# Kernel optimization log

Hardware: AMD Instinct MI355X
Metric: run time of the kernel (lower is better)

Reference implementation:

```python
import jax, jax.numpy as jnp
import numpy as np

DIM = 768
NH = 12
HID = int(DIM * 1.5)  # 1152
B_, T_, W_ = 8, 8, 14
HW = 14 * 14
N = HW + 1
BT = B_ * T_


def _ln(x, g, b, eps=1e-5):
    m = jnp.mean(x, axis=-1, keepdims=True)
    v = jnp.var(x, axis=-1, keepdims=True)
    return (x - m) / jnp.sqrt(v + eps) * g + b


def _attn(x, wqkv, wproj, bproj, nh):
    # manual q@k^T -> softmax -> @v, as in the torch module (no qkv bias)
    b, n, c = x.shape
    hd = c // nh
    scale = hd ** -0.5
    qkv = (x @ wqkv.T).reshape(b, n, 3, nh, hd).transpose(2, 0, 3, 1, 4)
    q, k, v = qkv[0], qkv[1], qkv[2]
    a = jax.nn.softmax(jnp.einsum('bhnd,bhmd->bhnm', q, k) * scale, axis=-1)
    o = jnp.einsum('bhnm,bhmd->bhnd', a, v).transpose(0, 2, 1, 3).reshape(b, n, c)
    return o @ wproj.T + bproj


def setup_inputs() -> dict:
    key = jax.random.key(0)
    ks = jax.random.split(key, 16)
    s = 0.02
    d = {
        'x': jax.random.normal(ks[0], (BT, N, DIM), jnp.float32),
        'ln1_g': jnp.ones((DIM,), jnp.float32),
        'ln1_b': jnp.zeros((DIM,), jnp.float32),
        'qkv_w': jax.random.normal(ks[1], (3 * DIM, DIM), jnp.float32) * s,
        'proj_w': jax.random.normal(ks[2], (DIM, DIM), jnp.float32) * s,
        'proj_b': jnp.zeros((DIM,), jnp.float32),
        'tln_g': jnp.ones((DIM,), jnp.float32),
        'tln_b': jnp.zeros((DIM,), jnp.float32),
        'tqkv_w': jax.random.normal(ks[3], (3 * DIM, DIM), jnp.float32) * s,
        'tproj_w': jax.random.normal(ks[4], (DIM, DIM), jnp.float32) * s,
        'tproj_b': jnp.zeros((DIM,), jnp.float32),
        # module zero-inits temporal_fc; use small random so the branch is exercised
        'tfc_w': jax.random.normal(ks[5], (DIM, DIM), jnp.float32) * s,
        'tfc_b': jnp.zeros((DIM,), jnp.float32),
        'ln2_g': jnp.ones((DIM,), jnp.float32),
        'ln2_b': jnp.zeros((DIM,), jnp.float32),
        'fc1_w': jax.random.normal(ks[6], (HID, DIM), jnp.float32) * s,
        'fc1_b': jnp.zeros((HID,), jnp.float32),
        'fc2_w': jax.random.normal(ks[7], (DIM, HID), jnp.float32) * s,
        'fc2_b': jnp.zeros((DIM,), jnp.float32),
        'B': B_, 'T': T_, 'W': W_,
    }
    return d


def reference(x, ln1_g, ln1_b, qkv_w, proj_w, proj_b,
              tln_g, tln_b, tqkv_w, tproj_w, tproj_b, tfc_w, tfc_b,
              ln2_g, ln2_b, fc1_w, fc1_b, fc2_w, fc2_b, B, T, W):
    bt, n, c = x.shape
    hw = n - 1  # spatial tokens (cls excluded)
    # temporal branch: (b t) hw m -> (b hw) t m
    xt = x[:, 1:, :].reshape(B, T, hw, c).transpose(0, 2, 1, 3).reshape(B * hw, T, c)
    xt = _attn(_ln(xt, tln_g, tln_b), tqkv_w, tproj_w, tproj_b, NH)
    xt = xt.reshape(B, hw, T, c).transpose(0, 2, 1, 3).reshape(bt, hw, c)
    xt = xt @ tfc_w.T + tfc_b
    x = x.at[:, 1:, :].add(xt)  # in-place += in torch
    # spatial attention + residual
    x = x + _attn(_ln(x, ln1_g, ln1_b), qkv_w, proj_w, proj_b, NH)
    # MLP + residual (exact GELU, matching nn.GELU default)
    h = jax.nn.gelu(_ln(x, ln2_g, ln2_b) @ fc1_w.T + fc1_b, approximate=False)
    x = x + (h @ fc2_w.T + fc2_b)
    return x
```

## Files before the change

kernel.cpp:

```cpp
#include <hip/hip_runtime.h>
#include <hip/hip_bf16.h>


#define DIM   768
#define NH    12
#define HD    64
#define HID   1152
#define HIDP  1280
#define B_    8
#define T_    8
#define HW_   196
#define NTOK  197
#define BT_   64
#define MROWS (BT_ * NTOK)
#define TROWS (B_ * HW_ * T_)

typedef __bf16 bf16x8 __attribute__((ext_vector_type(8)));
typedef float  f32x4  __attribute__((ext_vector_type(4)));

__device__ inline float bf2f(ushort u) { return __uint_as_float(((unsigned)u) << 16); }
__device__ inline ushort f2bf(float f) {
    unsigned u = __float_as_uint(f);
    unsigned r = (u + 0x7fffu + ((u >> 16) & 1u)) >> 16;
    return (ushort)r;
}

__device__ inline float wred_sum(float v) {
    #pragma unroll
    for (int m = 32; m; m >>= 1) v += __shfl_xor(v, m);
    return v;
}

__device__ __forceinline__ void gload_lds16(const void* g, void* l) {
    __builtin_amdgcn_global_load_lds(
        (const __attribute__((address_space(1))) unsigned int*)g,
        (__attribute__((address_space(3))) unsigned int*)l, 16, 0, 0);
}

__device__ __forceinline__ int xcd_lin(int gid, int nwg) {
    int q = nwg >> 3, r = nwg & 7;
    int xcd = gid & 7, idx = gid >> 3;
    return (xcd < r ? xcd * (q + 1) : r * (q + 1) + (xcd - r) * q) + idx;
}

#define MFMA16(a, b, c) __builtin_amdgcn_mfma_f32_16x16x32_bf16(a, b, c, 0, 0, 0)

#define PREP_T0 576
#define PREP_T1 (PREP_T0 + 192)
#define PREP_T2 (PREP_T1 + TROWS / 4)
#define FL_DD8  73728
#define FL_C0   (3 * FL_DD8)
#define FL_C1   (FL_C0 + FL_DD8)
#define FL_C2   (FL_C1 + 3 * FL_DD8)
#define FL_C3   (FL_C2 + FL_DD8)
#define FL_C4   (FL_C3 + HID * DIM / 8)
#define FL_C5   (FL_C4 + (HIDP - HID) * DIM / 8)
#define FL_C6   (FL_C5 + DIM * HIDP / 8)
#define FL_C7   (FL_C6 + HIDP / 8)
#define FL_C8   (FL_C7 + BT_ * DIM / 8)
#define PREP_GRID (PREP_T2 + (FL_C8 + 255) / 256)

__global__ __launch_bounds__(256) void prep(
    const float* __restrict__ x, const float* __restrict__ tln_g, const float* __restrict__ tln_b,
    const float* __restrict__ qkv_w, const float* __restrict__ proj_w,
    const float* __restrict__ tqkv_w, const float* __restrict__ tproj_w,
    const float* __restrict__ tproj_b, const float* __restrict__ tfc_wf,
    const float* __restrict__ tfc_b, const float* __restrict__ fc1_w,
    const float* __restrict__ fc1_b, const float* __restrict__ fc2_w,
    ushort* __restrict__ w_qkv, ushort* __restrict__ w_proj,
    ushort* __restrict__ w_tqkv, ushort* __restrict__ w_tfc,
    ushort* __restrict__ tprojT, ushort* __restrict__ w_fc1p,
    ushort* __restrict__ w_fc2p, float* __restrict__ fc1_bp,
    float* __restrict__ b_comb, ushort* __restrict__ bufA, float* __restrict__ out)
{
    __shared__ float tsm[32][33];
    int b = blockIdx.x, tid = threadIdx.x;

    if (b < PREP_T0) {
        int bx = b % 24, by = b / 24;
        int lx = tid & 31, ly = tid >> 5;
        #pragma unroll
        for (int i = 0; i < 32; i += 8)
            tsm[ly + i][lx] = tproj_w[(size_t)(by * 32 + ly + i) * DIM + bx * 32 + lx];
        __syncthreads();
        #pragma unroll
        for (int i = 0; i < 32; i += 8)
            tprojT[(size_t)(bx * 32 + ly + i) * DIM + by * 32 + lx] = f2bf(tsm[lx][ly + i]);
        return;
    }
    if (b < PREP_T1) {
        int w = (b - PREP_T0) * 4 + (tid >> 6), lane = tid & 63;
        float s = 0.f;
        for (int j = lane; j < DIM; j += 64) s += tfc_wf[(size_t)w * DIM + j] * tproj_b[j];
        s = wred_sum(s);
        if (lane == 0) b_comb[w] = s + tfc_b[w];
        return;
    }
    if (b < PREP_T2) {
        int widx = tid >> 6, lane = tid & 63;
        int r = (b - PREP_T1) * 4 + widx;
        int t = r & 7, pp = (r >> 3) % HW_, bb = r / (HW_ * T_);
        const float* row = x + ((size_t)(bb * T_ + t) * NTOK + 1 + pp) * DIM;
        float v[12], sum = 0.f, sq = 0.f;
        #pragma unroll
        for (int c = 0; c < 3; ++c) {
            float4 t4 = *(const float4*)(row + c * 256 + lane * 4);
            v[c*4+0] = t4.x; v[c*4+1] = t4.y; v[c*4+2] = t4.z; v[c*4+3] = t4.w;
            sum += t4.x + t4.y + t4.z + t4.w;
            sq  += t4.x*t4.x + t4.y*t4.y + t4.z*t4.z + t4.w*t4.w;
        }
        sum = wred_sum(sum); sq = wred_sum(sq);
        float mean = sum * (1.f / DIM);
        float var  = sq * (1.f / DIM) - mean * mean;
        float rstd = rsqrtf(var + 1e-5f);
        #pragma unroll
        for (int c = 0; c < 3; ++c) {
            int idx = c * 256 + lane * 4;
            float4 gg = *(const float4*)(tln_g + idx);
            float4 bb2 = *(const float4*)(tln_b + idx);
            ushort4 o;
            o.x = f2bf((v[c*4+0] - mean) * rstd * gg.x + bb2.x);
            o.y = f2bf((v[c*4+1] - mean) * rstd * gg.y + bb2.y);
            o.z = f2bf((v[c*4+2] - mean) * rstd * gg.z + bb2.z);
            o.w = f2bf((v[c*4+3] - mean) * rstd * gg.w + bb2.w);
            *(ushort4*)(bufA + (size_t)r * DIM + idx) = o;
        }
        return;
    }

    int i = (b - PREP_T2) * 256 + tid;
    if (i >= FL_C8) return;
    if (i < FL_C4) {
        const float* s; ushort* d; int base;
        if      (i < FL_C0) { s = qkv_w;  d = w_qkv;  base = 0;     }
        else if (i < FL_C1) { s = proj_w; d = w_proj; base = FL_C0; }
        else if (i < FL_C2) { s = tqkv_w; d = w_tqkv; base = FL_C1; }
        else if (i < FL_C3) { s = tfc_wf; d = w_tfc;  base = FL_C2; }
        else                { s = fc1_w;  d = w_fc1p; base = FL_C3; }
        int k = i - base;
        float4 a = *(const float4*)(s + (size_t)k * 8);
        float4 bb = *(const float4*)(s + (size_t)k * 8 + 4);
        ushort o[8] = {f2bf(a.x), f2bf(a.y), f2bf(a.z), f2bf(a.w),
                       f2bf(bb.x), f2bf(bb.y), f2bf(bb.z), f2bf(bb.w)};
        *(uint4*)(d + (size_t)k * 8) = *(const uint4*)o;
    } else if (i < FL_C5) {
        int k = i - FL_C4;
        uint4 z = {0u, 0u, 0u, 0u};
        *(uint4*)(w_fc1p + (size_t)HID * DIM + (size_t)k * 8) = z;
    } else if (i < FL_C6) {
        int k = i - FL_C5;
        int r = k / (HIDP / 8), c8 = (k % (HIDP / 8)) * 8;
        ushort o[8];
        if (c8 < HID) {
            const float* s = fc2_w + (size_t)r * HID + c8;
            #pragma unroll
            for (int e = 0; e < 8; ++e) o[e] = f2bf(s[e]);
        } else {
            #pragma unroll
            for (int e = 0; e < 8; ++e) o[e] = 0;
        }
        *(uint4*)(w_fc2p + (size_t)r * HIDP + c8) = *(const uint4*)o;
    } else if (i < FL_C7) {
        int k = (i - FL_C6) * 8;
        #pragma unroll
        for (int e = 0; e < 8; ++e) fc1_bp[k + e] = (k + e < HID) ? fc1_b[k + e] : 0.f;
    } else {
        int k = (i - FL_C7) * 8;
        int r = k / DIM, c = k % DIM;
        size_t off = (size_t)r * NTOK * DIM + c;
        *(float4*)(out + off)     = *(const float4*)(x + off);
        *(float4*)(out + off + 4) = *(const float4*)(x + off + 4);
    }
}

enum { EPI_STORE = 0, EPI_BIAS_GELU = 1, EPI_BIAS_ADD = 2, EPI_INIT_TFC = 3 };

template <int KK, int EPI>
__global__ __launch_bounds__(512, 1) void gemm256(
    const ushort* __restrict__ Ag, const ushort* __restrict__ Wg,
    const float* __restrict__ bias, ushort* __restrict__ Cg,
    const float* __restrict__ xsrc, float* __restrict__ xf,
    int M, int N, int nm, int nn, int grp,
    const ushort* A2, const ushort* W2, ushort* C2,
    int M2, int N2, int nm2, int nn2, int split)
{
    __shared__ ushort As[2][256 * 64];
    __shared__ ushort Bs[2][256 * 64];

    const int tid  = threadIdx.x;
    const int lane = tid & 63, wid = tid >> 6;
    const int wr = wid >> 2, wc = wid & 3;
    const int fr = lane & 15, fq = lane >> 4;

    int bid = blockIdx.x;
    if (bid >= split) {
        Ag = A2; Wg = W2; Cg = C2; M = M2; N = N2; nm = nm2; nn = nn2;
        bid -= split;
    }

    int lin = xcd_lin(bid, nm * nn);
    int per = grp * nn;
    int g2 = lin / per, rem = lin % per;
    int bm = g2 * grp;
    int gm = nm - bm; if (gm > grp) gm = grp;
    const int m0 = (bm + rem % gm) * 256;
    const int n0 = (rem / gm) * 256;

    const int srow = wid * 8 + (lane >> 3);
    const int scol = 8 * ((lane & 7) ^ (lane >> 3));
    const ushort* aP[4]; const ushort* bP[4];
    #pragma unroll
    for (int j = 0; j < 4; ++j) {
        int ra = m0 + j * 64 + srow; if (ra >= M) ra = M - 1;
        aP[j] = Ag + (size_t)ra * KK + scol;
        bP[j] = Wg + (size_t)(n0 + j * 64 + srow) * KK + scol;
    }
    const int ldso = (wid * 8) * 64;

    f32x4 acc[8][4] = {};
    bf16x8 af[4][2], b0[2][2], b1[2][2];

    const int sw0 = (fq * 8) ^ ((fr & 7) * 8);
    const int sw1 = (32 + fq * 8) ^ ((fr & 7) * 8);

    #pragma unroll
    for (int j = 0; j < 4; ++j) gload_lds16(aP[j], &As[0][j * 4096 + ldso]);
    #pragma unroll
    for (int j = 0; j < 4; ++j) gload_lds16(bP[j], &Bs[0][j * 4096 + ldso]);

    constexpr int NT = KK / 64;
    #pragma unroll
    for (int t = 0; t < NT; ++t) {
        const int rb = t & 1, wb = rb ^ 1;
        const bool st = (t + 1 < NT);
        const int kw = (t + 1) * 64;

        asm volatile("s_waitcnt vmcnt(0)" ::: "memory");
        __builtin_amdgcn_s_barrier();
        __builtin_amdgcn_sched_barrier(0);

        #pragma unroll
        for (int mf = 0; mf < 4; ++mf) {
            af[mf][0] = *(const bf16x8*)&As[rb][(wr * 128 + mf * 16 + fr) * 64 + sw0];
            af[mf][1] = *(const bf16x8*)&As[rb][(wr * 128 + mf * 16 + fr) * 64 + sw1];
        }
        #pragma unroll
        for (int nf = 0; nf < 2; ++nf) {
            b0[nf][0] = *(const bf16x8*)&Bs[rb][(wc * 64 + nf * 16 + fr) * 64 + sw0];
            b0[nf][1] = *(const bf16x8*)&Bs[rb][(wc * 64 + nf * 16 + fr) * 64 + sw1];
        }
        if (st) {
            #pragma unroll
            for (int j = 0; j < 4; ++j) gload_lds16(aP[j] + kw, &As[wb][j * 4096 + ldso]);
        }
        asm volatile("s_waitcnt lgkmcnt(0)" ::: "memory");
        __builtin_amdgcn_sched_barrier(0);
        __builtin_amdgcn_s_setprio(1);
        #pragma unroll
        for (int mf = 0; mf < 4; ++mf)
            #pragma unroll
            for (int nf = 0; nf < 2; ++nf) {
                acc[mf][nf] = MFMA16(af[mf][0], b0[nf][0], acc[mf][nf]);
                acc[mf][nf] = MFMA16(af[mf][1], b0[nf][1], acc[mf][nf]);
            }
        __builtin_amdgcn_s_setprio(0);
        __builtin_amdgcn_sched_barrier(0);

        #pragma unroll
        for (int nf = 0; nf < 2; ++nf) {
            b1[nf][0] = *(const bf16x8*)&Bs[rb][(wc * 64 + (nf + 2) * 16 + fr) * 64 + sw0];
            b1[nf][1] = *(const bf16x8*)&Bs[rb][(wc * 64 + (nf + 2) * 16 + fr) * 64 + sw1];
        }
        if (st) {
            #pragma unroll
            for (int j = 0; j < 4; ++j) gload_lds16(bP[j] + kw, &Bs[wb][j * 4096 + ldso]);
        }
        asm volatile("s_waitcnt lgkmcnt(0)" ::: "memory");
        __builtin_amdgcn_sched_barrier(0);
        __builtin_amdgcn_s_setprio(1);
        #pragma unroll
        for (int mf = 0; mf < 4; ++mf)
            #pragma unroll
            for (int nf = 0; nf < 2; ++nf) {
                acc[mf][nf + 2] = MFMA16(af[mf][0], b1[nf][0], acc[mf][nf + 2]);
                acc[mf][nf + 2] = MFMA16(af[mf][1], b1[nf][1], acc[mf][nf + 2]);
            }
        __builtin_amdgcn_s_setprio(0);
        __builtin_amdgcn_sched_barrier(0);

        #pragma unroll
        for (int mf = 0; mf < 4; ++mf) {
            af[mf][0] = *(const bf16x8*)&As[rb][(wr * 128 + 64 + mf * 16 + fr) * 64 + sw0];
            af[mf][1] = *(const bf16x8*)&As[rb][(wr * 128 + 64 + mf * 16 + fr) * 64 + sw1];
        }
        asm volatile("s_waitcnt lgkmcnt(0)" ::: "memory");
        __builtin_amdgcn_sched_barrier(0);
        __builtin_amdgcn_s_setprio(1);
        #pragma unroll
        for (int mf = 0; mf < 4; ++mf)
            #pragma unroll
            for (int nf = 0; nf < 2; ++nf) {
                acc[mf + 4][nf] = MFMA16(af[mf][0], b0[nf][0], acc[mf + 4][nf]);
                acc[mf + 4][nf] = MFMA16(af[mf][1], b0[nf][1], acc[mf + 4][nf]);
            }
        __builtin_amdgcn_s_setprio(0);
        __builtin_amdgcn_sched_barrier(0);

        __builtin_amdgcn_s_setprio(1);
        #pragma unroll
        for (int mf = 0; mf < 4; ++mf)
            #pragma unroll
            for (int nf = 0; nf < 2; ++nf) {
                acc[mf + 4][nf + 2] = MFMA16(af[mf][0], b1[nf][0], acc[mf + 4][nf + 2]);
                acc[mf + 4][nf + 2] = MFMA16(af[mf][1], b1[nf][1], acc[mf + 4][nf + 2]);
            }
        __builtin_amdgcn_s_setprio(0);
        __builtin_amdgcn_sched_barrier(0);
    }

    #pragma unroll
    for (int mf = 0; mf < 8; ++mf)
        #pragma unroll
        for (int e = 0; e < 4; ++e) {
            int row = m0 + wr * 128 + mf * 16 + fq * 4 + e;
            if (row >= M) continue;
            size_t dstrow = 0;
            if constexpr (EPI == EPI_INIT_TFC) {
                int t2 = row & 7, pp = (row >> 3) % HW_, bb = row / (HW_ * T_);
                dstrow = ((size_t)(bb * T_ + t2) * NTOK + 1 + pp) * DIM;
            }
            #pragma unroll
            for (int nf = 0; nf < 4; ++nf) {
                int col = n0 + wc * 64 + nf * 16 + fr;
                float v = acc[mf][nf][e];
                if constexpr (EPI != EPI_STORE) v += bias[col];
                if constexpr (EPI == EPI_BIAS_GELU) v = 0.5f * v * (1.0f + erff(v * 0.70710678118654752f));
                if constexpr (EPI == EPI_STORE || EPI == EPI_BIAS_GELU) {
                    Cg[(size_t)row * N + col] = f2bf(v);
                } else if constexpr (EPI == EPI_BIAS_ADD) {
                    xf[(size_t)row * DIM + col] += v;
                } else {
                    xf[dstrow + col] = xsrc[dstrow + col] + v;
                }
            }
        }
}

__global__ __launch_bounds__(256) void ln_f32(
    const float* __restrict__ src, const float* __restrict__ g,
    const float* __restrict__ b, ushort* __restrict__ dst, int rows)
{
    int widx = threadIdx.x >> 6, lane = threadIdx.x & 63;
    int r = blockIdx.x * 4 + widx;
    if (r >= rows) return;
    const float* row = src + (size_t)r * DIM;
    float v[12], sum = 0.f, sq = 0.f;
    #pragma unroll
    for (int c = 0; c < 3; ++c) {
        float4 t = *(const float4*)(row + c * 256 + lane * 4);
        v[c*4+0] = t.x; v[c*4+1] = t.y; v[c*4+2] = t.z; v[c*4+3] = t.w;
        sum += t.x + t.y + t.z + t.w;
        sq  += t.x*t.x + t.y*t.y + t.z*t.z + t.w*t.w;
    }
    sum = wred_sum(sum); sq = wred_sum(sq);
    float mean = sum * (1.f / DIM);
    float var  = sq * (1.f / DIM) - mean * mean;
    float rstd = rsqrtf(var + 1e-5f);
    #pragma unroll
    for (int c = 0; c < 3; ++c) {
        int idx = c * 256 + lane * 4;
        float4 gg = *(const float4*)(g + idx);
        float4 bb = *(const float4*)(b + idx);
        ushort4 o;
        o.x = f2bf((v[c*4+0] - mean) * rstd * gg.x + bb.x);
        o.y = f2bf((v[c*4+1] - mean) * rstd * gg.y + bb.y);
        o.z = f2bf((v[c*4+2] - mean) * rstd * gg.z + bb.z);
        o.w = f2bf((v[c*4+3] - mean) * rstd * gg.w + bb.w);
        *(ushort4*)(dst + (size_t)r * DIM + idx) = o;
    }
}

__global__ __launch_bounds__(256) void attn_temporal(
    const ushort* __restrict__ qkv, ushort* __restrict__ O)
{
    int widx = threadIdx.x >> 6, lane = threadIdx.x & 63;
    int w = blockIdx.x * 4 + widx;
    int s = w / NH, h = w % NH;
    int qi = lane >> 3, kj = lane & 7;

    const ushort* qrow = qkv + (size_t)(s * 8 + qi) * (3 * DIM) + h * HD;
    const ushort* krow = qkv + (size_t)(s * 8 + kj) * (3 * DIM) + DIM + h * HD;
    float d = 0.f;
    #pragma unroll
    for (int c = 0; c < 8; ++c) {
        uint4 qa = *(const uint4*)(qrow + c * 8);
        uint4 ka = *(const uint4*)(krow + c * 8);
        const ushort* qs = (const ushort*)&qa;
        const ushort* ks = (const ushort*)&ka;
        #pragma unroll
        for (int e = 0; e < 8; ++e) d += bf2f(qs[e]) * bf2f(ks[e]);
    }
    float sc = d * 0.125f;
    float mx = sc;
    #pragma unroll
    for (int m = 4; m; m >>= 1) mx = fmaxf(mx, __shfl_xor(mx, m));
    float p = expf(sc - mx);
    float sum = p;
    #pragma unroll
    for (int m = 4; m; m >>= 1) sum += __shfl_xor(sum, m);
    p /= sum;

    float o[8] = {};
    int base = lane & ~7;
    #pragma unroll
    for (int t = 0; t < 8; ++t) {
        float pt = __shfl(p, base + t);
        const ushort* vrow = qkv + (size_t)(s * 8 + t) * (3 * DIM) + 2 * DIM + h * HD + kj * 8;
        uint4 va = *(const uint4*)vrow;
        const ushort* vs = (const ushort*)&va;
        #pragma unroll
        for (int e = 0; e < 8; ++e) o[e] += pt * bf2f(vs[e]);
    }
    ushort out[8];
    #pragma unroll
    for (int e = 0; e < 8; ++e) out[e] = f2bf(o[e]);
    *(uint4*)(O + (size_t)(s * 8 + qi) * DIM + h * HD + kj * 8) = *(const uint4*)out;
}

#define KS_STRIDE 72
#define VT_STRIDE 208
#define P_STRIDE  208
#define KS_OFF    0
#define VT_OFF    (197 * KS_STRIDE)
#define P_OFF     (VT_OFF + 64 * VT_STRIDE)
#define LDS_TOT   (P_OFF + 4 * 16 * P_STRIDE)

__global__ __launch_bounds__(256, 2) void attn_spatial_mfma(
    const ushort* __restrict__ qkv, ushort* __restrict__ O)
{
    __shared__ ushort lds[LDS_TOT];
    const int tid = threadIdx.x, lane = tid & 63, wid = tid >> 6;
    const int fr = lane & 15, fq = lane >> 4;
    int lin = xcd_lin(blockIdx.x, BT_ * NH);
    const int s = lin / NH, h = lin % NH;
    const size_t base = (size_t)s * NTOK * (3 * DIM);
    const ushort* Qg = qkv + base + h * HD;
    const ushort* Kg = qkv + base + DIM + h * HD;
    const ushort* Vg = qkv + base + 2 * DIM + h * HD;

    for (int chunk = tid; chunk < NTOK * 8; chunk += 256) {
        int r = chunk >> 3, c = (chunk & 7) * 8;
        uint4 v = *(const uint4*)(Kg + (size_t)r * (3 * DIM) + c);
        *(uint4*)&lds[KS_OFF + r * KS_STRIDE + c] = v;
    }
    for (int chunk = tid; chunk < 208 * 8; chunk += 256) {
        int k = chunk >> 3, c = (chunk & 7) * 8;
        uint4 v = {0u, 0u, 0u, 0u};
        if (k < NTOK) v = *(const uint4*)(Vg + (size_t)k * (3 * DIM) + c);
        const ushort* e = (const ushort*)&v;
        #pragma unroll
        for (int j = 0; j < 8; ++j) lds[VT_OFF + (c + j) * VT_STRIDE + k] = e[j];
    }
    __syncthreads();

    ushort* P = &lds[P_OFF + wid * 16 * P_STRIDE];

    for (int qi = wid; qi < 13; qi += 4) {
        int qrow = qi * 16 + fr; if (qrow > NTOK - 1) qrow = NTOK - 1;
        bf16x8 qf0 = *(const bf16x8*)(Qg + (size_t)qrow * (3 * DIM) + fq * 8);
        bf16x8 qf1 = *(const bf16x8*)(Qg + (size_t)qrow * (3 * DIM) + 32 + fq * 8);

        f32x4 sacc[13];
        #pragma unroll
        for (int t = 0; t < 13; ++t) {
            bf16x8 kf0 = *(const bf16x8*)&lds[KS_OFF + (t * 16 + fr) * KS_STRIDE + fq * 8];
            bf16x8 kf1 = *(const bf16x8*)&lds[KS_OFF + (t * 16 + fr) * KS_STRIDE + 32 + fq * 8];
            f32x4 z = {0.f, 0.f, 0.f, 0.f};
            z = MFMA16(kf0, qf0, z);
            sacc[t] = MFMA16(kf1, qf1, z);
        }

        float m = -1e30f;
        #pragma unroll
        for (int t = 0; t < 13; ++t)
            #pragma unroll
            for (int e = 0; e < 4; ++e) {
                int k = t * 16 + fq * 4 + e;
                float v = (k < NTOK) ? sacc[t][e] * 0.125f : -1e30f;
                sacc[t][e] = v;
                m = fmaxf(m, v);
            }
        m = fmaxf(m, __shfl_xor(m, 16));
        m = fmaxf(m, __shfl_xor(m, 32));
        float sum = 0.f;
        #pragma unroll
        for (int t = 0; t < 13; ++t)
            #pragma unroll
            for (int e = 0; e < 4; ++e) {
                float p = expf(sacc[t][e] - m);
                sacc[t][e] = p;
                sum += p;
            }
        sum += __shfl_xor(sum, 16);
        sum += __shfl_xor(sum, 32);
        float rd = 1.f / sum;

        #pragma unroll
        for (int t = 0; t < 13; ++t) {
            ushort2 w0 = { f2bf(sacc[t][0] * rd), f2bf(sacc[t][1] * rd) };
            ushort2 w1 = { f2bf(sacc[t][2] * rd), f2bf(sacc[t][3] * rd) };
            *(ushort2*)&P[fr * P_STRIDE + t * 16 + fq * 4]     = w0;
            *(ushort2*)&P[fr * P_STRIDE + t * 16 + fq * 4 + 2] = w1;
        }

        f32x4 oacc[4] = {};
        #pragma unroll
        for (int st = 0; st < 6; ++st) {
            bf16x8 pf = *(const bf16x8*)&P[fr * P_STRIDE + st * 32 + fq * 8];
            #pragma unroll
            for (int dt = 0; dt < 4; ++dt) {
                bf16x8 vf = *(const bf16x8*)&lds[VT_OFF + (dt * 16 + fr) * VT_STRIDE + st * 32 + fq * 8];
                oacc[dt] = MFMA16(pf, vf, oacc[dt]);
            }
        }
        {
            bf16x8 zz = {};
            bf16x8 pf = zz;
            if (fq < 2) pf = *(const bf16x8*)&P[fr * P_STRIDE + 192 + fq * 8];
            #pragma unroll
            for (int dt = 0; dt < 4; ++dt) {
                bf16x8 vf = zz;
                if (fq < 2) vf = *(const bf16x8*)&lds[VT_OFF + (dt * 16 + fr) * VT_STRIDE + 192 + fq * 8];
                oacc[dt] = MFMA16(pf, vf, oacc[dt]);
            }
        }

        #pragma unroll
        for (int dt = 0; dt < 4; ++dt)
            #pragma unroll
            for (int e = 0; e < 4; ++e) {
                int q = qi * 16 + fq * 4 + e;
                if (q < NTOK)
                    O[(size_t)(s * NTOK + q) * DIM + h * HD + dt * 16 + fr] = f2bf(oacc[dt][e]);
            }
    }
}

extern "C" void kernel_launch(void* const* d_in, const int* in_sizes, int n_in,
                              void* d_out, int out_size, void* d_ws, size_t ws_size,
                              hipStream_t stream)
{
    const float* x      = (const float*)d_in[0];
    const float* ln1_g  = (const float*)d_in[1];
    const float* ln1_b  = (const float*)d_in[2];
    const float* qkv_w  = (const float*)d_in[3];
    const float* proj_w = (const float*)d_in[4];
    const float* proj_b = (const float*)d_in[5];
    const float* tln_g  = (const float*)d_in[6];
    const float* tln_b  = (const float*)d_in[7];
    const float* tqkv_w = (const float*)d_in[8];
    const float* tproj_w= (const float*)d_in[9];
    const float* tproj_b= (const float*)d_in[10];
    const float* tfc_w  = (const float*)d_in[11];
    const float* tfc_b  = (const float*)d_in[12];
    const float* ln2_g  = (const float*)d_in[13];
    const float* ln2_b  = (const float*)d_in[14];
    const float* fc1_w  = (const float*)d_in[15];
    const float* fc1_b  = (const float*)d_in[16];
    const float* fc2_w  = (const float*)d_in[17];
    const float* fc2_b  = (const float*)d_in[18];

    float* out = (float*)d_out;

    char* p = (char*)d_ws;
    ushort* w_qkv  = (ushort*)p; p += (size_t)(3*DIM*DIM) * 2;
    ushort* w_proj = (ushort*)p; p += (size_t)(DIM*DIM) * 2;
    ushort* w_tqkv = (ushort*)p; p += (size_t)(3*DIM*DIM) * 2;
    ushort* w_tfc  = (ushort*)p; p += (size_t)(DIM*DIM) * 2;
    ushort* tprojT = (ushort*)p; p += (size_t)(DIM*DIM) * 2;
    ushort* w_comb = (ushort*)p; p += (size_t)(DIM*DIM) * 2;
    ushort* w_fc1p = (ushort*)p; p += (size_t)(HIDP*DIM) * 2;
    ushort* w_fc2p = (ushort*)p; p += (size_t)(DIM*HIDP) * 2;
    float*  b_comb = (float*)p;  p += DIM * 4;
    float*  fc1_bp = (float*)p;  p += HIDP * 4;
    ushort* bufA   = (ushort*)p; p += (size_t)MROWS * DIM * 2;
    ushort* bufC   = (ushort*)p; p += (size_t)MROWS * DIM * 2;
    ushort* bufB   = (ushort*)p;

    prep<<<dim3(PREP_GRID), dim3(256), 0, stream>>>(
        x, tln_g, tln_b, qkv_w, proj_w, tqkv_w, tproj_w, tproj_b,
        tfc_w, tfc_b, fc1_w, fc1_b, fc2_w,
        w_qkv, w_proj, w_tqkv, w_tfc, tprojT, w_fc1p, w_fc2p,
        fc1_bp, b_comb, bufA, out);

    #define GEMM256(KV, EPI, A, W, BIAS, C, XS, XF, M, N, GRP) \
        gemm256<KV, EPI><<<dim3((((M) + 255) / 256) * ((N) / 256)), dim3(512), 0, stream>>>( \
            A, W, BIAS, C, XS, XF, M, N, ((M) + 255) / 256, (N) / 256, GRP, \
            nullptr, nullptr, nullptr, 0, 0, 0, 0, 0x7fffffff)

    {
        int nm = (TROWS + 255) / 256, nn = (3 * DIM) / 256;
        int split = nm * nn;
        gemm256<DIM, EPI_STORE><<<dim3(split + 9), dim3(512), 0, stream>>>(
            bufA, w_tqkv, nullptr, bufB, nullptr, nullptr, TROWS, 3 * DIM, nm, nn, 1,
            w_tfc, tprojT, w_comb, DIM, DIM, 3, 3, split);
    }
    attn_temporal<<<dim3(TROWS * NH / 8 / 4), dim3(256), 0, stream>>>(bufB, bufC);
    GEMM256(DIM, EPI_INIT_TFC, bufC, w_comb, b_comb, nullptr, x, out, TROWS, DIM, 1);

    ln_f32<<<dim3((MROWS + 3) / 4), dim3(256), 0, stream>>>(out, ln1_g, ln1_b, bufA, MROWS);
    GEMM256(DIM, EPI_STORE, bufA, w_qkv, nullptr, bufB, nullptr, nullptr, MROWS, 3 * DIM, 1);
    attn_spatial_mfma<<<dim3(BT_ * NH), dim3(256), 0, stream>>>(bufB, bufC);
    GEMM256(DIM, EPI_BIAS_ADD, bufC, w_proj, proj_b, nullptr, nullptr, out, MROWS, DIM, 1);

    ln_f32<<<dim3((MROWS + 3) / 4), dim3(256), 0, stream>>>(out, ln2_g, ln2_b, bufA, MROWS);
    GEMM256(DIM, EPI_BIAS_GELU, bufA, w_fc1p, fc1_bp, bufB, nullptr, nullptr, MROWS, HIDP, 1);
    GEMM256(HIDP, EPI_BIAS_ADD, bufB, w_fc2p, fc2_b, nullptr, nullptr, out, MROWS, DIM, 1);
    #undef GEMM256
}
```

Measured before the change: 376.1 us.

## Load full LDS tile once per k-step and skip padded K in fc2

The GEMM inner loop now loads all A and B fragments for the k-tile into registers up front, issues both global prefetches together, and runs all 64 MFMAs in one block. This replaces four interleaved load/compute phases with separate lgkmcnt waits. A separate leading-dimension template parameter lets the fc2 GEMM loop over K=1152 while keeping stride 1280, so it drops the padded zero columns. The cost is more live fragment registers and less overlap between LDS reads and MFMA issue.

```diff
diff --git a/kernel.cpp b/kernel.cpp
--- a/kernel.cpp
+++ b/kernel.cpp
@@ -175,7 +175,7 @@
 
 enum { EPI_STORE = 0, EPI_BIAS_GELU = 1, EPI_BIAS_ADD = 2, EPI_INIT_TFC = 3 };
 
-template <int KK, int EPI>
+template <int KK, int LD, int EPI>
 __global__ __launch_bounds__(512, 1) void gemm256(
     const ushort* __restrict__ Ag, const ushort* __restrict__ Wg,
     const float* __restrict__ bias, ushort* __restrict__ Cg,
@@ -212,13 +212,13 @@
     #pragma unroll
     for (int j = 0; j < 4; ++j) {
         int ra = m0 + j * 64 + srow; if (ra >= M) ra = M - 1;
-        aP[j] = Ag + (size_t)ra * KK + scol;
-        bP[j] = Wg + (size_t)(n0 + j * 64 + srow) * KK + scol;
+        aP[j] = Ag + (size_t)ra * LD + scol;
+        bP[j] = Wg + (size_t)(n0 + j * 64 + srow) * LD + scol;
     }
     const int ldso = (wid * 8) * 64;
 
     f32x4 acc[8][4] = {};
-    bf16x8 af[4][2], b0[2][2], b1[2][2];
+    bf16x8 a[8][2], b[4][2];
 
     const int sw0 = (fq * 8) ^ ((fr & 7) * 8);
     const int sw1 = (32 + fq * 8) ^ ((fr & 7) * 8);
@@ -240,79 +240,32 @@
         __builtin_amdgcn_sched_barrier(0);
 
         #pragma unroll
-        for (int mf = 0; mf < 4; ++mf) {
-            af[mf][0] = *(const bf16x8*)&As[rb][(wr * 128 + mf * 16 + fr) * 64 + sw0];
-            af[mf][1] = *(const bf16x8*)&As[rb][(wr * 128 + mf * 16 + fr) * 64 + sw1];
-        }
-        #pragma unroll
-        for (int nf = 0; nf < 2; ++nf) {
-            b0[nf][0] = *(const bf16x8*)&Bs[rb][(wc * 64 + nf * 16 + fr) * 64 + sw0];
-            b0[nf][1] = *(const bf16x8*)&Bs[rb][(wc * 64 + nf * 16 + fr) * 64 + sw1];
-        }
+        for (int mf = 0; mf < 8; ++mf) {
+            a[mf][0] = *(const bf16x8*)&As[rb][(wr * 128 + mf * 16 + fr) * 64 + sw0];
+            a[mf][1] = *(const bf16x8*)&As[rb][(wr * 128 + mf * 16 + fr) * 64 + sw1];
+        }
+        #pragma unroll
+        for (int nf = 0; nf < 4; ++nf) {
+            b[nf][0] = *(const bf16x8*)&Bs[rb][(wc * 64 + nf * 16 + fr) * 64 + sw0];
+            b[nf][1] = *(const bf16x8*)&Bs[rb][(wc * 64 + nf * 16 + fr) * 64 + sw1];
+        }
+        __builtin_amdgcn_sched_barrier(0);
+
         if (st) {
             #pragma unroll
             for (int j = 0; j < 4; ++j) gload_lds16(aP[j] + kw, &As[wb][j * 4096 + ldso]);
-        }
-        asm volatile("s_waitcnt lgkmcnt(0)" ::: "memory");
+            #pragma unroll
+            for (int j = 0; j < 4; ++j) gload_lds16(bP[j] + kw, &Bs[wb][j * 4096 + ldso]);
+        }
         __builtin_amdgcn_sched_barrier(0);
+
         __builtin_amdgcn_s_setprio(1);
         #pragma unroll
-        for (int mf = 0; mf < 4; ++mf)
-            #pragma unroll
-            for (int nf = 0; nf < 2; ++nf) {
-                acc[mf][nf] = MFMA16(af[mf][0], b0[nf][0], acc[mf][nf]);
-                acc[mf][nf] = MFMA16(af[mf][1], b0[nf][1], acc[mf][nf]);
-            }
-        __builtin_amdgcn_s_setprio(0);
-        __builtin_amdgcn_sched_barrier(0);
-
-        #pragma unroll
-        for (int nf = 0; nf < 2; ++nf) {
-            b1[nf][0] = *(const bf16x8*)&Bs[rb][(wc * 64 + (nf + 2) * 16 + fr) * 64 + sw0];
-            b1[nf][1] = *(const bf16x8*)&Bs[rb][(wc * 64 + (nf + 2) * 16 + fr) * 64 + sw1];
-        }
-        if (st) {
-            #pragma unroll
-            for (int j = 0; j < 4; ++j) gload_lds16(bP[j] + kw, &Bs[wb][j * 4096 + ldso]);
-        }
-        asm volatile("s_waitcnt lgkmcnt(0)" ::: "memory");
-        __builtin_amdgcn_sched_barrier(0);
-        __builtin_amdgcn_s_setprio(1);
-        #pragma unroll
-        for (int mf = 0; mf < 4; ++mf)
-            #pragma unroll
-            for (int nf = 0; nf < 2; ++nf) {
-                acc[mf][nf + 2] = MFMA16(af[mf][0], b1[nf][0], acc[mf][nf + 2]);
-                acc[mf][nf + 2] = MFMA16(af[mf][1], b1[nf][1], acc[mf][nf + 2]);
-            }
-        __builtin_amdgcn_s_setprio(0);
-        __builtin_amdgcn_sched_barrier(0);
-
-        #pragma unroll
-        for (int mf = 0; mf < 4; ++mf) {
-            af[mf][0] = *(const bf16x8*)&As[rb][(wr * 128 + 64 + mf * 16 + fr) * 64 + sw0];
-            af[mf][1] = *(const bf16x8*)&As[rb][(wr * 128 + 64 + mf * 16 + fr) * 64 + sw1];
-        }
-        asm volatile("s_waitcnt lgkmcnt(0)" ::: "memory");
-        __builtin_amdgcn_sched_barrier(0);
-        __builtin_amdgcn_s_setprio(1);
-        #pragma unroll
-        for (int mf = 0; mf < 4; ++mf)
-            #pragma unroll
-            for (int nf = 0; nf < 2; ++nf) {
-                acc[mf + 4][nf] = MFMA16(af[mf][0], b0[nf][0], acc[mf + 4][nf]);
-                acc[mf + 4][nf] = MFMA16(af[mf][1], b0[nf][1], acc[mf + 4][nf]);
-            }
-        __builtin_amdgcn_s_setprio(0);
-        __builtin_amdgcn_sched_barrier(0);
-
-        __builtin_amdgcn_s_setprio(1);
-        #pragma unroll
-        for (int mf = 0; mf < 4; ++mf)
-            #pragma unroll
-            for (int nf = 0; nf < 2; ++nf) {
-                acc[mf + 4][nf + 2] = MFMA16(af[mf][0], b1[nf][0], acc[mf + 4][nf + 2]);
-                acc[mf + 4][nf + 2] = MFMA16(af[mf][1], b1[nf][1], acc[mf + 4][nf + 2]);
+        for (int mf = 0; mf < 8; ++mf)
+            #pragma unroll
+            for (int nf = 0; nf < 4; ++nf) {
+                acc[mf][nf] = MFMA16(a[mf][0], b[nf][0], acc[mf][nf]);
+                acc[mf][nf] = MFMA16(a[mf][1], b[nf][1], acc[mf][nf]);
             }
         __builtin_amdgcn_s_setprio(0);
         __builtin_amdgcn_sched_barrier(0);
@@ -593,28 +546,28 @@
         w_qkv, w_proj, w_tqkv, w_tfc, tprojT, w_fc1p, w_fc2p,
         fc1_bp, b_comb, bufA, out);
 
-    #define GEMM256(KV, EPI, A, W, BIAS, C, XS, XF, M, N, GRP) \
-        gemm256<KV, EPI><<<dim3((((M) + 255) / 256) * ((N) / 256)), dim3(512), 0, stream>>>( \
+    #define GEMM256(KV, LDV, EPI, A, W, BIAS, C, XS, XF, M, N, GRP) \
+        gemm256<KV, LDV, EPI><<<dim3((((M) + 255) / 256) * ((N) / 256)), dim3(512), 0, stream>>>( \
             A, W, BIAS, C, XS, XF, M, N, ((M) + 255) / 256, (N) / 256, GRP, \
             nullptr, nullptr, nullptr, 0, 0, 0, 0, 0x7fffffff)
 
     {
         int nm = (TROWS + 255) / 256, nn = (3 * DIM) / 256;
         int split = nm * nn;
-        gemm256<DIM, EPI_STORE><<<dim3(split + 9), dim3(512), 0, stream>>>(
+        gemm256<DIM, DIM, EPI_STORE><<<dim3(split + 9), dim3(512), 0, stream>>>(
             bufA, w_tqkv, nullptr, bufB, nullptr, nullptr, TROWS, 3 * DIM, nm, nn, 1,
             w_tfc, tprojT, w_comb, DIM, DIM, 3, 3, split);
     }
     attn_temporal<<<dim3(TROWS * NH / 8 / 4), dim3(256), 0, stream>>>(bufB, bufC);
-    GEMM256(DIM, EPI_INIT_TFC, bufC, w_comb, b_comb, nullptr, x, out, TROWS, DIM, 1);
+    GEMM256(DIM, DIM, EPI_INIT_TFC, bufC, w_comb, b_comb, nullptr, x, out, TROWS, DIM, 1);
 
     ln_f32<<<dim3((MROWS + 3) / 4), dim3(256), 0, stream>>>(out, ln1_g, ln1_b, bufA, MROWS);
-    GEMM256(DIM, EPI_STORE, bufA, w_qkv, nullptr, bufB, nullptr, nullptr, MROWS, 3 * DIM, 1);
+    GEMM256(DIM, DIM, EPI_STORE, bufA, w_qkv, nullptr, bufB, nullptr, nullptr, MROWS, 3 * DIM, 1);
     attn_spatial_mfma<<<dim3(BT_ * NH), dim3(256), 0, stream>>>(bufB, bufC);
-    GEMM256(DIM, EPI_BIAS_ADD, bufC, w_proj, proj_b, nullptr, nullptr, out, MROWS, DIM, 1);
+    GEMM256(DIM, DIM, EPI_BIAS_ADD, bufC, w_proj, proj_b, nullptr, nullptr, out, MROWS, DIM, 1);
 
     ln_f32<<<dim3((MROWS + 3) / 4), dim3(256), 0, stream>>>(out, ln2_g, ln2_b, bufA, MROWS);
-    GEMM256(DIM, EPI_BIAS_GELU, bufA, w_fc1p, fc1_bp, bufB, nullptr, nullptr, MROWS, HIDP, 1);
-    GEMM256(HIDP, EPI_BIAS_ADD, bufB, w_fc2p, fc2_b, nullptr, nullptr, out, MROWS, DIM, 1);
+    GEMM256(DIM, DIM, EPI_BIAS_GELU, bufA, w_fc1p, fc1_bp, bufB, nullptr, nullptr, MROWS, HIDP, 1);
+    GEMM256(HID, HIDP, EPI_BIAS_ADD, bufB, w_fc2p, fc2_b, nullptr, nullptr, out, MROWS, DIM, 1);
     #undef GEMM256
 }
```

After: 396.4 us. 5.4% more time.
